# Optimization experiments

Hardware: AMD Instinct MI355X
Metric: run time of the kernel (lower is better)

The kernel has to match this reference:

```python
import jax, jax.numpy as jnp
import numpy as np

ALPHA = 0.2  # LeakyReLU negative slope
OUT_FEATURES = 64


def dsn2(t):
    # Closed-form doubly-stochastic normalization for one [N, N] slice.
    n = t.shape[0]
    rs = t.sum(axis=1, keepdims=True)          # [N, 1] row sums
    cs = t.sum(axis=0, keepdims=True)          # [1, N] col sums
    lamb = jnp.maximum(rs.max(), cs.max())
    r = n * lamb - t.sum()
    tt = t + (lamb * lamb - lamb * (rs + cs) + rs * cs) / r
    ttm = tt / tt.sum(axis=0)[0]               # divide by first column-sum (scalar), per original
    return jnp.where(t > 0, ttm, t)


def setup_inputs() -> dict:
    key = jax.random.key(0)
    k1, k2, k3, k4 = jax.random.split(key, 4)
    N, P, IN, OUT = 3072, 4, 256, OUT_FEATURES
    h = jax.random.normal(k1, (N, IN), dtype=jnp.float32)
    edge_attr = jax.random.uniform(k2, (P, N, N), dtype=jnp.float32)
    W = jax.random.normal(k3, (IN, OUT), dtype=jnp.float32) * 0.1
    a = jax.random.normal(k4, (2 * OUT, 1), dtype=jnp.float32) * 0.1
    return {"h": h, "edge_attr": edge_attr, "W": W, "a": a}


def reference(h, edge_attr, W, a):
    F = OUT_FEATURES
    Wh = h @ W                                   # [N, F]
    Wh1 = Wh @ a[:F, :]                          # [N, 1]
    Wh2 = Wh @ a[F:, :]                          # [N, 1]
    e = jax.nn.leaky_relu(Wh1 + Wh2.T, negative_slope=ALPHA)  # [N, N]
    e = e * edge_attr                            # [P, N, N]
    attention = jax.vmap(dsn2)(e)                # [P, N, N]
    h_prime = jnp.einsum('pij,jf->pif', attention, Wh)  # [P, N, F]
    # concat=True: cat along feature dim -> [N, P*F]
    N = h.shape[0]
    h_cat = jnp.transpose(h_prime, (1, 0, 2)).reshape(N, -1)
    return jax.nn.elu(h_cat), e
```

## Files before the change

kernel.cpp:

```cpp
#include <hip/hip_runtime.h>
#include <math.h>

#define NN 3072
#define PP 4
#define INF_ 256
#define FF 64
#define LEAK 0.2f
#define KB2 96

#define WH1_OFF  0
#define WH2_OFF  (WH1_OFF + NN)
#define RS_OFF   (WH2_OFF + NN)
#define CS_OFF   (RS_OFF + PP * NN)
#define U_OFF    (CS_OFF + PP * NN)
#define V_OFF    (U_OFF + PP * NN)
#define SCAL_OFF (V_OFF + PP * NN)
#define WHT_OFF  (SCAL_OFF + 8)
#define CP_OFF   (WHT_OFF + (NN * FF) / 2)

typedef short short8 __attribute__((ext_vector_type(8)));
typedef float floatx4 __attribute__((ext_vector_type(4)));

__device__ inline unsigned short f2bf(float x) {
    unsigned u = __float_as_uint(x);
    return (unsigned short)((u + 0x7FFFu + ((u >> 16) & 1u)) >> 16);
}

__global__ __launch_bounds__(64) void k1_gemm(const float* __restrict__ h,
                                              const float* __restrict__ W,
                                              const float* __restrict__ a,
                                              float* __restrict__ ws) {
    int row = blockIdx.x;
    int f = threadIdx.x;
    __shared__ float hrow[INF_];
    ((float4*)hrow)[f] = ((const float4*)(h + (size_t)row * INF_))[f];
    __syncthreads();
    float acc = 0.f;
#pragma unroll 8
    for (int k = 0; k < INF_; ++k) acc = fmaf(hrow[k], W[k * FF + f], acc);
    unsigned short* whT = (unsigned short*)(ws + WHT_OFF);
    whT[(size_t)f * NN + row] = f2bf(acc);
    float s1 = acc * a[f];
    float s2 = acc * a[FF + f];
#pragma unroll
    for (int off = 32; off > 0; off >>= 1) {
        s1 += __shfl_down(s1, off);
        s2 += __shfl_down(s2, off);
    }
    if (f == 0) { ws[WH1_OFF + row] = s1; ws[WH2_OFF + row] = s2; }
}

__global__ __launch_bounds__(256) void k2_e(const float* __restrict__ edge,
                                            float* __restrict__ e_out,
                                            float* __restrict__ ws) {
    int p = blockIdx.y;
    int row0 = blockIdx.x * 32;
    int tid = threadIdx.x;
    const float* Wh1 = ws + WH1_OFF;
    const float4* Wh2v = (const float4*)(ws + WH2_OFF);
    float4 wv[3];
#pragma unroll
    for (int c = 0; c < 3; ++c) wv[c] = Wh2v[c * 256 + tid];
    float colAcc[12];
#pragma unroll
    for (int i = 0; i < 12; ++i) colAcc[i] = 0.f;
    __shared__ float rowpart[32][4];
    const size_t slice = (size_t)p * NN * NN;
    for (int r = 0; r < 32; ++r) {
        int row = row0 + r;
        float w1 = Wh1[row];
        const float4* ein = (const float4*)(edge + slice + (size_t)row * NN);
        float4* eout = (float4*)(e_out + slice + (size_t)row * NN);
        float racc = 0.f;
#pragma unroll
        for (int c = 0; c < 3; ++c) {
            int j4 = c * 256 + tid;
            float4 ea = ein[j4];
            float4 w = wv[c];
            float4 ev;
            float b;
            b = w1 + w.x; b = b > 0.f ? b : LEAK * b; ev.x = b * ea.x;
            b = w1 + w.y; b = b > 0.f ? b : LEAK * b; ev.y = b * ea.y;
            b = w1 + w.z; b = b > 0.f ? b : LEAK * b; ev.z = b * ea.z;
            b = w1 + w.w; b = b > 0.f ? b : LEAK * b; ev.w = b * ea.w;
            eout[j4] = ev;
            colAcc[c * 4 + 0] += ev.x; colAcc[c * 4 + 1] += ev.y;
            colAcc[c * 4 + 2] += ev.z; colAcc[c * 4 + 3] += ev.w;
            racc += (ev.x + ev.y) + (ev.z + ev.w);
        }
#pragma unroll
        for (int off = 32; off > 0; off >>= 1) racc += __shfl_down(racc, off);
        if ((tid & 63) == 0) rowpart[r][tid >> 6] = racc;
    }
    __syncthreads();
    if (tid < 128) {
        float vv = rowpart[tid >> 2][tid & 3];
        vv += __shfl_down(vv, 2);
        vv += __shfl_down(vv, 1);
        if ((tid & 3) == 0) ws[RS_OFF + p * NN + row0 + (tid >> 2)] = vv;
    }
    float4* cp = (float4*)(ws + CP_OFF + (size_t)(p * KB2 + blockIdx.x) * NN);
#pragma unroll
    for (int c = 0; c < 3; ++c) {
        float4 cv;
        cv.x = colAcc[c * 4 + 0]; cv.y = colAcc[c * 4 + 1];
        cv.z = colAcc[c * 4 + 2]; cv.w = colAcc[c * 4 + 3];
        cp[c * 256 + tid] = cv;
    }
}

__global__ __launch_bounds__(256) void k3a_red(float* __restrict__ ws) {
    int p = blockIdx.y;
    int col = blockIdx.x * 256 + threadIdx.x;
    const float* cp = ws + CP_OFF + (size_t)p * KB2 * NN + col;
    float s = 0.f;
#pragma unroll 4
    for (int b = 0; b < KB2; ++b) s += cp[(size_t)b * NN];
    ws[CS_OFF + p * NN + col] = s;
}

__global__ __launch_bounds__(256) void k3b_scal(float* __restrict__ ws) {
    int p = blockIdx.x;
    int tid = threadIdx.x;
    const float* rs = ws + RS_OFF + p * NN;
    const float* cs = ws + CS_OFF + p * NN;
    float mx = -3.4e38f, sum = 0.f;
    for (int i = tid; i < NN; i += 256) {
        float rv = rs[i], cv = cs[i];
        mx = fmaxf(mx, fmaxf(rv, cv));
        sum += rv;
    }
#pragma unroll
    for (int off = 32; off > 0; off >>= 1) {
        mx = fmaxf(mx, __shfl_down(mx, off));
        sum += __shfl_down(sum, off);
    }
    __shared__ float smx[4], ssum[4];
    __shared__ float s_lamb, s_invlr;
    if ((tid & 63) == 0) { smx[tid >> 6] = mx; ssum[tid >> 6] = sum; }
    __syncthreads();
    if (tid == 0) {
        float lamb = fmaxf(fmaxf(smx[0], smx[1]), fmaxf(smx[2], smx[3]));
        float T = ssum[0] + ssum[1] + ssum[2] + ssum[3];
        float r = (float)NN * lamb - T;
        s_lamb = lamb;
        s_invlr = 1.f / (r * lamb);
        ws[SCAL_OFF + p] = 1.f / lamb;
    }
    __syncthreads();
    float lamb = s_lamb, invlr = s_invlr;
    for (int i = tid; i < NN; i += 256) {
        ws[U_OFF + p * NN + i] = (lamb - rs[i]) * invlr;
        ws[V_OFF + p * NN + i] = lamb - cs[i];
    }
}

__global__ __launch_bounds__(64) void k4_mfma(const float* __restrict__ e_in,
                                              const float* __restrict__ ws,
                                              float* __restrict__ out0) {
    int p = blockIdx.y;
    int row0 = blockIdx.x * 16;
    int tid = threadIdx.x;
    __shared__ __align__(16) unsigned short sA[16][56];
    __shared__ __align__(16) unsigned short sB[64][56];
    const unsigned short* whT = (const unsigned short*)(ws + WHT_OFF);
    const float* u = ws + U_OFF + p * NN;
    const float* v = ws + V_OFF + p * NN;
    float invl = ws[SCAL_OFF + p];
    const float* eslice = e_in + (size_t)p * NN * NN;

    int arow = tid >> 2;
    int kg = tid & 3;
    float u_r = u[row0 + arow];
    const float4* erow = (const float4*)(eslice + (size_t)(row0 + arow) * NN);
    const float4* vrow = (const float4*)v;
    const int4* wrow = (const int4*)(whT + (size_t)tid * NN);

    floatx4 acc[4];
#pragma unroll
    for (int nt = 0; nt < 4; ++nt)
#pragma unroll
        for (int i = 0; i < 4; ++i) acc[nt][i] = 0.f;

    float4 e0, e1, v0, v1;
    int4 b0, b1, b2, b3;
    auto ldg = [&](int k0) {
        int idx = (k0 >> 2) + kg * 2;
        e0 = erow[idx]; e1 = erow[idx + 1];
        v0 = vrow[idx]; v1 = vrow[idx + 1];
        int widx = k0 >> 3;
        b0 = wrow[widx]; b1 = wrow[widx + 1]; b2 = wrow[widx + 2]; b3 = wrow[widx + 3];
    };
    ldg(0);
    for (int k0 = 0; k0 < NN; k0 += 32) {
        float a0 = e0.x > 0.f ? fmaf(u_r, v0.x, e0.x * invl) : e0.x;
        float a1 = e0.y > 0.f ? fmaf(u_r, v0.y, e0.y * invl) : e0.y;
        float a2 = e0.z > 0.f ? fmaf(u_r, v0.z, e0.z * invl) : e0.z;
        float a3 = e0.w > 0.f ? fmaf(u_r, v0.w, e0.w * invl) : e0.w;
        float a4 = e1.x > 0.f ? fmaf(u_r, v1.x, e1.x * invl) : e1.x;
        float a5 = e1.y > 0.f ? fmaf(u_r, v1.y, e1.y * invl) : e1.y;
        float a6 = e1.z > 0.f ? fmaf(u_r, v1.z, e1.z * invl) : e1.z;
        float a7 = e1.w > 0.f ? fmaf(u_r, v1.w, e1.w * invl) : e1.w;
        int4 pa;
        pa.x = (int)f2bf(a0) | ((int)f2bf(a1) << 16);
        pa.y = (int)f2bf(a2) | ((int)f2bf(a3) << 16);
        pa.z = (int)f2bf(a4) | ((int)f2bf(a5) << 16);
        pa.w = (int)f2bf(a6) | ((int)f2bf(a7) << 16);
        *(int4*)&sA[arow][kg * 8] = pa;
        *(int4*)&sB[tid][0]  = b0;
        *(int4*)&sB[tid][8]  = b1;
        *(int4*)&sB[tid][16] = b2;
        *(int4*)&sB[tid][24] = b3;
        __syncthreads();
        if (k0 + 32 < NN) ldg(k0 + 32);
        int mrow = tid & 15;
        int kq = tid >> 4;
        short8 af = *(const short8*)&sA[mrow][kq * 8];
#pragma unroll
        for (int nt = 0; nt < 4; ++nt) {
            short8 bf = *(const short8*)&sB[nt * 16 + mrow][kq * 8];
            acc[nt] = __builtin_amdgcn_mfma_f32_16x16x32_bf16(af, bf, acc[nt], 0, 0, 0);
        }
        __syncthreads();
    }
#pragma unroll
    for (int nt = 0; nt < 4; ++nt)
#pragma unroll
        for (int r = 0; r < 4; ++r) {
            float x = acc[nt][r];
            x = x > 0.f ? x : (expf(x) - 1.0f);
            int orow = row0 + (tid >> 4) * 4 + r;
            out0[(size_t)orow * (PP * FF) + p * FF + nt * 16 + (tid & 15)] = x;
        }
}

extern "C" void kernel_launch(void* const* d_in, const int* in_sizes, int n_in,
                              void* d_out, int out_size, void* d_ws, size_t ws_size,
                              hipStream_t stream) {
    const float* h    = (const float*)d_in[0];
    const float* edge = (const float*)d_in[1];
    const float* W    = (const float*)d_in[2];
    const float* a    = (const float*)d_in[3];
    float* out0  = (float*)d_out;
    float* e_out = out0 + (size_t)NN * PP * FF;
    float* ws = (float*)d_ws;

    k1_gemm<<<NN, 64, 0, stream>>>(h, W, a, ws);
    k2_e<<<dim3(NN / 32, PP), 256, 0, stream>>>(edge, e_out, ws);
    k3a_red<<<dim3(NN / 256, PP), 256, 0, stream>>>(ws);
    k3b_scal<<<PP, 256, 0, stream>>>(ws);
    k4_mfma<<<dim3(NN / 16, PP), 64, 0, stream>>>(e_out, ws, out0);
}
```

Measured before the change: 399.4 us.

## Split-K the attention GEMM and shrink row tiles in edge kernel

The MFMA aggregation kernel now splits the K dimension into four chunks via a third grid axis. Each chunk writes fp32 partials to workspace, and a new reduction kernel sums them and applies ELU. The edge kernel processes 8 rows per block instead of 32, and the column-sum reduction is split across four warps with a shared-memory combine. Both changes aim to raise the number of blocks in flight, at the cost of extra partial-sum traffic and one more launch.

```diff
diff --git a/kernel.cpp b/kernel.cpp
--- a/kernel.cpp
+++ b/kernel.cpp
@@ -6,7 +6,10 @@
 #define INF_ 256
 #define FF 64
 #define LEAK 0.2f
-#define KB2 96
+#define KB2 384
+#define KS 4
+#define KCH (NN / KS)
+#define PNF (PP * NN * FF)
 
 #define WH1_OFF  0
 #define WH2_OFF  (WH1_OFF + NN)
@@ -54,7 +57,7 @@
                                             float* __restrict__ e_out,
                                             float* __restrict__ ws) {
     int p = blockIdx.y;
-    int row0 = blockIdx.x * 32;
+    int row0 = blockIdx.x * 8;
     int tid = threadIdx.x;
     const float* Wh1 = ws + WH1_OFF;
     const float4* Wh2v = (const float4*)(ws + WH2_OFF);
@@ -64,9 +67,10 @@
     float colAcc[12];
 #pragma unroll
     for (int i = 0; i < 12; ++i) colAcc[i] = 0.f;
-    __shared__ float rowpart[32][4];
+    __shared__ float rowpart[8][4];
     const size_t slice = (size_t)p * NN * NN;
-    for (int r = 0; r < 32; ++r) {
+#pragma unroll 2
+    for (int r = 0; r < 8; ++r) {
         int row = row0 + r;
         float w1 = Wh1[row];
         const float4* ein = (const float4*)(edge + slice + (size_t)row * NN);
@@ -93,7 +97,7 @@
         if ((tid & 63) == 0) rowpart[r][tid >> 6] = racc;
     }
     __syncthreads();
-    if (tid < 128) {
+    if (tid < 32) {
         float vv = rowpart[tid >> 2][tid & 3];
         vv += __shfl_down(vv, 2);
         vv += __shfl_down(vv, 1);
@@ -111,12 +115,20 @@
 
 __global__ __launch_bounds__(256) void k3a_red(float* __restrict__ ws) {
     int p = blockIdx.y;
-    int col = blockIdx.x * 256 + threadIdx.x;
-    const float* cp = ws + CP_OFF + (size_t)p * KB2 * NN + col;
+    int col = blockIdx.x * 64 + (threadIdx.x & 63);
+    int chunk = threadIdx.x >> 6;
+    const float* cp = ws + CP_OFF + (size_t)p * KB2 * NN + (size_t)chunk * 96 * NN + col;
     float s = 0.f;
-#pragma unroll 4
-    for (int b = 0; b < KB2; ++b) s += cp[(size_t)b * NN];
-    ws[CS_OFF + p * NN + col] = s;
+#pragma unroll 8
+    for (int b = 0; b < 96; ++b) s += cp[(size_t)b * NN];
+    __shared__ float sred[4][64];
+    sred[chunk][threadIdx.x & 63] = s;
+    __syncthreads();
+    if (threadIdx.x < 64) {
+        float t = sred[0][threadIdx.x] + sred[1][threadIdx.x] +
+                  sred[2][threadIdx.x] + sred[3][threadIdx.x];
+        ws[CS_OFF + p * NN + col] = t;
+    }
 }
 
 __global__ __launch_bounds__(256) void k3b_scal(float* __restrict__ ws) {
@@ -156,9 +168,9 @@
 }
 
 __global__ __launch_bounds__(64) void k4_mfma(const float* __restrict__ e_in,
-                                              const float* __restrict__ ws,
-                                              float* __restrict__ out0) {
+                                              float* __restrict__ ws) {
     int p = blockIdx.y;
+    int z = blockIdx.z;
     int row0 = blockIdx.x * 16;
     int tid = threadIdx.x;
     __shared__ __align__(16) unsigned short sA[16][56];
@@ -182,6 +194,7 @@
 #pragma unroll
         for (int i = 0; i < 4; ++i) acc[nt][i] = 0.f;
 
+    const int kbase = z * KCH;
     float4 e0, e1, v0, v1;
     int4 b0, b1, b2, b3;
     auto ldg = [&](int k0) {
@@ -191,8 +204,8 @@
         int widx = k0 >> 3;
         b0 = wrow[widx]; b1 = wrow[widx + 1]; b2 = wrow[widx + 2]; b3 = wrow[widx + 3];
     };
-    ldg(0);
-    for (int k0 = 0; k0 < NN; k0 += 32) {
+    ldg(kbase);
+    for (int k0 = kbase; k0 < kbase + KCH; k0 += 32) {
         float a0 = e0.x > 0.f ? fmaf(u_r, v0.x, e0.x * invl) : e0.x;
         float a1 = e0.y > 0.f ? fmaf(u_r, v0.y, e0.y * invl) : e0.y;
         float a2 = e0.z > 0.f ? fmaf(u_r, v0.z, e0.z * invl) : e0.z;
@@ -212,7 +225,7 @@
         *(int4*)&sB[tid][16] = b2;
         *(int4*)&sB[tid][24] = b3;
         __syncthreads();
-        if (k0 + 32 < NN) ldg(k0 + 32);
+        if (k0 + 32 < kbase + KCH) ldg(k0 + 32);
         int mrow = tid & 15;
         int kq = tid >> 4;
         short8 af = *(const short8*)&sA[mrow][kq * 8];
@@ -223,15 +236,26 @@
         }
         __syncthreads();
     }
+    float* part = ws + CP_OFF + (size_t)z * PNF + (size_t)p * NN * FF + (size_t)row0 * FF;
 #pragma unroll
     for (int nt = 0; nt < 4; ++nt)
 #pragma unroll
-        for (int r = 0; r < 4; ++r) {
-            float x = acc[nt][r];
-            x = x > 0.f ? x : (expf(x) - 1.0f);
-            int orow = row0 + (tid >> 4) * 4 + r;
-            out0[(size_t)orow * (PP * FF) + p * FF + nt * 16 + (tid & 15)] = x;
-        }
+        for (int r = 0; r < 4; ++r)
+            part[((tid >> 4) * 4 + r) * FF + nt * 16 + (tid & 15)] = acc[nt][r];
+}
+
+__global__ __launch_bounds__(256) void k5_red(const float* __restrict__ ws,
+                                              float* __restrict__ out0) {
+    int i = blockIdx.x * 256 + threadIdx.x;
+    const float* part = ws + CP_OFF;
+    float s = part[i] + part[PNF + i] + part[2 * PNF + i] + part[3 * (size_t)PNF + i];
+    s = s > 0.f ? s : (expf(s) - 1.0f);
+    int f = i & 63;
+    int n = (i >> 6) & (NN - 1);
+    int p = i >> 6 >> 11;
+    p = i / (NN * FF);
+    n = (i - p * NN * FF) >> 6;
+    out0[(size_t)n * (PP * FF) + p * FF + f] = s;
 }
 
 extern "C" void kernel_launch(void* const* d_in, const int* in_sizes, int n_in,
@@ -246,8 +270,9 @@
     float* ws = (float*)d_ws;
 
     k1_gemm<<<NN, 64, 0, stream>>>(h, W, a, ws);
-    k2_e<<<dim3(NN / 32, PP), 256, 0, stream>>>(edge, e_out, ws);
-    k3a_red<<<dim3(NN / 256, PP), 256, 0, stream>>>(ws);
+    k2_e<<<dim3(NN / 8, PP), 256, 0, stream>>>(edge, e_out, ws);
+    k3a_red<<<dim3(NN / 64, PP), 256, 0, stream>>>(ws);
     k3b_scal<<<PP, 256, 0, stream>>>(ws);
-    k4_mfma<<<dim3(NN / 16, PP), 64, 0, stream>>>(e_out, ws, out0);
-}
+    k4_mfma<<<dim3(NN / 16, PP, KS), 64, 0, stream>>>(e_out, ws);
+    k5_red<<<PNF / 256, 256, 0, stream>>>(ws, out0);
+}
```

Result: no change. 394.9 us (-1.1%).
